# Kernel optimization log

Hardware: AMD Instinct MI355X
Metric: run time of the kernel (lower is better)

Reference implementation:

```python
import jax, jax.numpy as jnp
import numpy as np

N_NODES = 65536
N_EDGES = 262144
N_GRAPHS = 2048
NF = 16   # num_node_features
EF = 6    # num_edge_features
H1, H2, H3 = 32, 16, 8  # conv1 out, conv2 out, lin1 out


def _lin_init(key, fan_in, fan_out):
    kw, kb = jax.random.split(key)
    s = 1.0 / np.sqrt(fan_in)
    w = jax.random.uniform(kw, (fan_in, fan_out), minval=-s, maxval=s, dtype=jnp.float32)
    b = jax.random.uniform(kb, (fan_out,), minval=-s, maxval=s, dtype=jnp.float32)
    return w, b


def setup_inputs() -> dict:
    key = jax.random.key(0)
    ks = jax.random.split(key, 16)
    inp = {}
    inp["x_p"] = jax.random.normal(ks[0], (N_NODES, NF), dtype=jnp.float32)
    inp["x_d"] = jax.random.normal(ks[1], (4, NF), dtype=jnp.float32)  # unused by forward
    inp["edge_attr_p"] = jax.random.uniform(ks[2], (N_EDGES, EF), dtype=jnp.float32)
    inp["edge_attr_d"] = jax.random.uniform(ks[3], (4, EF), dtype=jnp.float32)  # unused
    inp["edge_index_p"] = jax.random.randint(ks[4], (2, N_EDGES), 0, N_NODES, dtype=jnp.int32)
    inp["x_p_batch"] = jnp.sort(jax.random.randint(ks[5], (N_NODES,), 0, N_GRAPHS, dtype=jnp.int32))
    # conv1: NNConv(NF, 32); edge nn: Linear(EF,16) -> ReLU -> Linear(16, NF*32)
    inp["nn1_w1"], inp["nn1_b1"] = _lin_init(ks[6], EF, 16)
    inp["nn1_w2"], inp["nn1_b2"] = _lin_init(ks[7], 16, NF * H1)
    inp["root1"] = _lin_init(ks[8], NF, H1)[0]
    inp["bias1"] = jnp.zeros((H1,), dtype=jnp.float32)
    # conv2: NNConv(32, 16); edge nn: Linear(EF,16) -> ReLU -> Linear(16, 32*16)
    inp["nn2_w1"], inp["nn2_b1"] = _lin_init(ks[9], EF, 16)
    inp["nn2_w2"], inp["nn2_b2"] = _lin_init(ks[10], 16, H1 * H2)
    inp["root2"] = _lin_init(ks[11], H1, H2)[0]
    inp["bias2"] = jnp.zeros((H2,), dtype=jnp.float32)
    # attention pooling gate: Linear(NF,NF) -> ReLU -> Linear(NF,1)
    inp["gate_w1"], inp["gate_b1"] = _lin_init(ks[12], NF, NF)
    inp["gate_w2"], inp["gate_b2"] = _lin_init(ks[13], NF, 1)
    # head: Linear(16+16, 8) -> Linear(8, 1)  (attention=True)
    inp["lin1_w"], inp["lin1_b"] = _lin_init(ks[14], H2 + NF, H3)
    inp["lin2_w"], inp["lin2_b"] = _lin_init(ks[15], H3, 1)
    return inp


def _nnconv(x, edge_attr, src, dst, w1, b1, w2, b2, root, bias, in_c, out_c, n_nodes):
    # per-edge dynamic weight matrix Theta(e) : [E, in_c, out_c]
    h = jax.nn.relu(edge_attr @ w1 + b1) @ w2 + b2
    w_dyn = h.reshape(-1, in_c, out_c)
    msg = jnp.einsum('ei,eio->eo', x[src], w_dyn)          # [E, out_c]
    agg = jax.ops.segment_sum(msg, dst, num_segments=n_nodes)  # scatter-add
    return agg + x @ root + bias


def _attention_pool(x, batch, gw1, gb1, gw2, gb2, n_graphs):
    g = (jax.nn.relu(x @ gw1 + gb1) @ gw2 + gb2)[:, 0]     # [N] gate logits
    m = jax.ops.segment_max(g, batch, num_segments=n_graphs)
    e = jnp.exp(g - m[batch])
    s = jax.ops.segment_sum(e, batch, num_segments=n_graphs)
    alpha = e / s[batch]                                    # per-graph softmax
    return jax.ops.segment_sum(alpha[:, None] * x, batch, num_segments=n_graphs)


def _mean_pool(x, batch, n_graphs):
    s = jax.ops.segment_sum(x, batch, num_segments=n_graphs)
    cnt = jax.ops.segment_sum(jnp.ones((x.shape[0],), x.dtype), batch, num_segments=n_graphs)
    return s / jnp.maximum(cnt, 1.0)[:, None]


def reference(x_p, x_d, edge_attr_p, edge_attr_d, edge_index_p, x_p_batch,
              nn1_w1, nn1_b1, nn1_w2, nn1_b2, root1, bias1,
              nn2_w1, nn2_b1, nn2_w2, nn2_b2, root2, bias2,
              gate_w1, gate_b1, gate_w2, gate_b2,
              lin1_w, lin1_b, lin2_w, lin2_b):
    src, dst = edge_index_p[0], edge_index_p[1]
    # attention pooling on raw node features (attention=True)
    x_att = _attention_pool(x_p, x_p_batch, gate_w1, gate_b1, gate_w2, gate_b2, N_GRAPHS)
    # two NNConv layers with ReLU
    h = jax.nn.relu(_nnconv(x_p, edge_attr_p, src, dst, nn1_w1, nn1_b1, nn1_w2, nn1_b2,
                            root1, bias1, NF, H1, N_NODES))
    h = jax.nn.relu(_nnconv(h, edge_attr_p, src, dst, nn2_w1, nn2_b1, nn2_w2, nn2_b2,
                            root2, bias2, H1, H2, N_NODES))
    g = _mean_pool(h, x_p_batch, N_GRAPHS)                  # [B, 16]
    g = jnp.concatenate([g, x_att], axis=1)                 # [B, 32]
    # dropout p=0.5 is identity in eval mode
    g = g @ lin1_w + lin1_b
    out = g @ lin2_w + lin2_b                               # [B, 1]
    return out
```

## Files before the change

### kernel.cpp

```cpp
#include <hip/hip_runtime.h>

#define NN 65536
#define NE 262144
#define NG 2048

typedef __attribute__((ext_vector_type(16))) float f32x16;
typedef __attribute__((ext_vector_type(4)))  float f32x4;
typedef __attribute__((ext_vector_type(8)))  __bf16 bf16x8;

__device__ inline unsigned pack2(float a, float b) {
    return __builtin_amdgcn_perm(__float_as_uint(b), __float_as_uint(a), 0x07060302u);
}
__device__ inline float lof(float p) {
    return p - __uint_as_float(__float_as_uint(p) & 0xffff0000u);
}
__device__ inline bf16x8 asb(uint4 u) { return __builtin_bit_cast(bf16x8, u); }

__global__ __launch_bounds__(256) void k_setup(
    const int* __restrict__ batch,
    const float* __restrict__ w2a, const float* __restrict__ b2a,
    const float* __restrict__ w2b, const float* __restrict__ b2c,
    int* __restrict__ cnt, int* __restrict__ cur, int* __restrict__ goffs,
    unsigned* __restrict__ f1, unsigned* __restrict__ f2)
{
    int t = blockIdx.x * 256 + threadIdx.x;
    if (t < NN) { cnt[t] = 0; cur[t] = 0; }
    if (t <= NG) {
        int lo = 0, hi = NN;
        while (lo < hi) {
            int mid = (lo + hi) >> 1;
            if (batch[mid] < t) lo = mid + 1; else hi = mid;
        }
        goffs[t] = lo;
    }
    if (t < 17408) {
        int c = t / 8704;
        int r = t - c * 8704;
        int d = r & 3;
        int l = (r >> 2) & 63;
        int tt = (r >> 8) & 1;
        int s = r >> 9;
        if (c == 0) {
            int n = l & 31, g = l >> 5;
            int j0 = 2*d;
            int c0 = (g*8 + j0)*32 + n;
            int c1 = c0 + 32;
            float a = (s < 16) ? w2a[s*512 + c0] : b2a[c0];
            float b = (s < 16) ? w2a[s*512 + c1] : b2a[c1];
            f1[r] = tt ? pack2(lof(a), lof(b)) : pack2(a, b);
        } else {
            int n = l & 15, g = l >> 4;
            int j0 = 2*d;
            int c0 = (g*8 + j0)*16 + n;
            int c1 = c0 + 16;
            float a = (s < 16) ? w2b[s*512 + c0] : b2c[c0];
            float b = (s < 16) ? w2b[s*512 + c1] : b2c[c1];
            f2[r] = tt ? pack2(lof(a), lof(b)) : pack2(a, b);
        }
    }
}

__global__ __launch_bounds__(64) void k_gateatt(const float* __restrict__ x,
    const float* __restrict__ gw1, const float* __restrict__ gb1,
    const float* __restrict__ gw2, const float* __restrict__ gb2,
    const int* __restrict__ goffs, float* __restrict__ x_att)
{
    __shared__ float sw[256];
    __shared__ float sb[16];
    __shared__ float sw2[16];
    __shared__ float sb2;
    __shared__ float gb[1024];
    const int g = blockIdx.x;
    const int lane = threadIdx.x;
    for (int i = lane; i < 256; i += 64) sw[i] = gw1[i];
    if (lane < 16) { sb[lane] = gb1[lane]; sw2[lane] = gw2[lane]; }
    if (lane == 0) sb2 = gb2[0];
    const int s = goffs[g], e = goffs[g + 1];
    const int cnt = e - s;
    if (cnt <= 0) {
        if (lane < 16) x_att[g*16 + lane] = 0.f;
        return;
    }
    const int cap = cnt < 1024 ? cnt : 1024;
    __syncthreads();
    for (int ii = lane; ii < cap; ii += 64) {
        const float4* xp = (const float4*)(x + (size_t)(s + ii) * 16);
        float xv[16];
#pragma unroll
        for (int i = 0; i < 4; ++i) {
            float4 tt = xp[i];
            xv[4*i] = tt.x; xv[4*i+1] = tt.y; xv[4*i+2] = tt.z; xv[4*i+3] = tt.w;
        }
        float gv = sb2;
#pragma unroll
        for (int j = 0; j < 16; ++j) {
            float a = sb[j];
#pragma unroll
            for (int i = 0; i < 16; ++i) a += xv[i] * sw[i*16 + j];
            gv += fmaxf(a, 0.f) * sw2[j];
        }
        gb[ii] = gv;
    }
    __syncthreads();
    float m = -1e30f;
    for (int ii = lane; ii < cap; ii += 64) m = fmaxf(m, gb[ii]);
#pragma unroll
    for (int d = 32; d; d >>= 1) m = fmaxf(m, __shfl_xor(m, d));
    float sum = 0.f;
    for (int ii = lane; ii < cap; ii += 64) {
        float ev = expf(gb[ii] - m);
        gb[ii] = ev;
        sum += ev;
    }
#pragma unroll
    for (int d = 32; d; d >>= 1) sum += __shfl_xor(sum, d);
    const float inv = 1.f / sum;
    __syncthreads();
    const int f = lane & 15, sub = lane >> 4;
    float acc = 0.f;
    for (int ii = sub; ii < cap; ii += 4)
        acc += gb[ii] * inv * x[(size_t)(s + ii)*16 + f];
    acc += __shfl_xor(acc, 16);
    acc += __shfl_xor(acc, 32);
    if (lane < 16) x_att[g*16 + f] = acc;
}

__global__ __launch_bounds__(256) void k_hist(const int* __restrict__ ei, int* __restrict__ cnt)
{
    int e = blockIdx.x * 256 + threadIdx.x;
    if (e >= NE) return;
    atomicAdd(&cnt[ei[NE + e]], 1);
}

__global__ __launch_bounds__(256) void k_scan_blk(const int* __restrict__ cnt,
    int* __restrict__ offs, int* __restrict__ bsum)
{
    __shared__ int s[256];
    int t = threadIdx.x, b = blockIdx.x;
    int v = cnt[b*256 + t];
    s[t] = v;
    __syncthreads();
#pragma unroll
    for (int d = 1; d < 256; d <<= 1) {
        int add = (t >= d) ? s[t - d] : 0;
        __syncthreads();
        s[t] += add;
        __syncthreads();
    }
    offs[b*256 + t] = s[t] - v;
    if (t == 255) bsum[b] = s[255];
}

__global__ __launch_bounds__(256) void k_scan_top(const int* __restrict__ bsum,
    int* __restrict__ boff)
{
    __shared__ int s[256];
    int t = threadIdx.x;
    int v = bsum[t];
    s[t] = v;
    __syncthreads();
#pragma unroll
    for (int d = 1; d < 256; d <<= 1) {
        int add = (t >= d) ? s[t - d] : 0;
        __syncthreads();
        s[t] += add;
        __syncthreads();
    }
    boff[t] = s[t] - v;
}

__global__ __launch_bounds__(256) void k_scan_add(int* __restrict__ offs,
    const int* __restrict__ boff)
{
    int i = blockIdx.x * 256 + threadIdx.x;
    if (i == 0) offs[NN] = NE;
    if (i >= NN) return;
    offs[i] += boff[i >> 8];
}

__global__ __launch_bounds__(256) void k_scatter(const int* __restrict__ ei,
    const int* __restrict__ offs, int* __restrict__ cur, int2* __restrict__ epair)
{
    int e = blockIdx.x * 256 + threadIdx.x;
    if (e >= NE) return;
    int d = ei[NE + e];
    int pos = offs[d] + atomicAdd(&cur[d], 1);
    epair[pos] = make_int2(e, ei[e]);
}

__global__ __launch_bounds__(256) void k_conv1(
    const float* __restrict__ x, const float* __restrict__ ea,
    const int2* __restrict__ epair,
    const float* __restrict__ w1, const float* __restrict__ b1,
    const unsigned* __restrict__ bfrag, float* __restrict__ msg)
{
    __shared__ uint4 s_tab[17*2*64];
    const int tid  = threadIdx.x;
    for (int i = tid; i < 17*2*64; i += 256) s_tab[i] = ((const uint4*)bfrag)[i];
    __syncthreads();
    const int lane = tid & 63;
    const int wid  = tid >> 6;
    const int m    = lane & 31;
    const int g    = lane >> 5;

    const int tile = blockIdx.x*4 + wid;
    const int p    = tile*32 + m;
    const int2 ep  = epair[p];
    const int e    = ep.x, src = ep.y;

    float xs[8];
    {
        const float4* xp = (const float4*)(x + (size_t)src*16 + g*8);
        float4 aa = xp[0], bb = xp[1];
        xs[0]=aa.x; xs[1]=aa.y; xs[2]=aa.z; xs[3]=aa.w;
        xs[4]=bb.x; xs[5]=bb.y; xs[6]=bb.z; xs[7]=bb.w;
    }
    float h[17];
    {
        const float2 e01 = *(const float2*)(ea + (size_t)e*6);
        const float2 e23 = *(const float2*)(ea + (size_t)e*6 + 2);
        const float2 e45 = *(const float2*)(ea + (size_t)e*6 + 4);
        const float a0=e01.x, a1=e01.y, a2=e23.x, a3=e23.y, a4=e45.x, a5=e45.y;
#pragma unroll
        for (int j = 0; j < 16; ++j) {
            float c = b1[j];
            c += a0*w1[0*16+j]; c += a1*w1[1*16+j]; c += a2*w1[2*16+j];
            c += a3*w1[3*16+j]; c += a4*w1[4*16+j]; c += a5*w1[5*16+j];
            h[j] = fmaxf(c, 0.f);
        }
        h[16] = 1.f;
    }

    f32x16 acc0 = {}, acc1 = {};
#pragma unroll
    for (int s = 0; s < 17; ++s) {
        const float hs = h[s];
        float p0 = hs*xs[0], p1 = hs*xs[1], p2 = hs*xs[2], p3 = hs*xs[3];
        float p4 = hs*xs[4], p5 = hs*xs[5], p6 = hs*xs[6], p7 = hs*xs[7];
        uint4 uh = { pack2(p0,p1), pack2(p2,p3), pack2(p4,p5), pack2(p6,p7) };
        uint4 ul = { pack2(lof(p0),lof(p1)), pack2(lof(p2),lof(p3)),
                     pack2(lof(p4),lof(p5)), pack2(lof(p6),lof(p7)) };
        uint4 wh = s_tab[(s*2+0)*64 + lane];
        uint4 wl = s_tab[(s*2+1)*64 + lane];
        if (s & 1) {
            acc1 = __builtin_amdgcn_mfma_f32_32x32x16_bf16(asb(uh), asb(wh), acc1, 0, 0, 0);
            acc1 = __builtin_amdgcn_mfma_f32_32x32x16_bf16(asb(uh), asb(wl), acc1, 0, 0, 0);
            acc1 = __builtin_amdgcn_mfma_f32_32x32x16_bf16(asb(ul), asb(wh), acc1, 0, 0, 0);
        } else {
            acc0 = __builtin_amdgcn_mfma_f32_32x32x16_bf16(asb(uh), asb(wh), acc0, 0, 0, 0);
            acc0 = __builtin_amdgcn_mfma_f32_32x32x16_bf16(asb(uh), asb(wl), acc0, 0, 0, 0);
            acc0 = __builtin_amdgcn_mfma_f32_32x32x16_bf16(asb(ul), asb(wh), acc0, 0, 0, 0);
        }
    }

    float* mbase = msg + (size_t)tile*32*32;
    const int rb = g*4;
#pragma unroll
    for (int r = 0; r < 16; ++r) {
        int mr = (r&3) + 8*(r>>2) + rb;
        mbase[(size_t)mr*32 + m] = acc0[r] + acc1[r];
    }
}

__global__ __launch_bounds__(256) void k_conv2(
    const float* __restrict__ x, const float* __restrict__ ea,
    const int2* __restrict__ epair,
    const float* __restrict__ w1, const float* __restrict__ b1,
    const unsigned* __restrict__ bfrag, float* __restrict__ msg)
{
    __shared__ uint4 s_tab[17*2*64];
    __shared__ float lt[4][16*21];
    const int tid  = threadIdx.x;
    for (int i = tid; i < 17*2*64; i += 256) s_tab[i] = ((const uint4*)bfrag)[i];
    __syncthreads();
    const int lane = tid & 63;
    const int wid  = tid >> 6;
    const int m    = lane & 15;
    const int g    = lane >> 4;

    const int tile = blockIdx.x*4 + wid;
    const int p    = tile*16 + m;
    const int2 ep  = epair[p];
    const int e    = ep.x, src = ep.y;

    uint4 xh, xl;
    {
        const float4* xp = (const float4*)(x + (size_t)src*32 + g*8);
        float4 aa = xp[0], bb = xp[1];
        xh = (uint4){ pack2(aa.x,aa.y), pack2(aa.z,aa.w), pack2(bb.x,bb.y), pack2(bb.z,bb.w) };
        xl = (uint4){ pack2(lof(aa.x),lof(aa.y)), pack2(lof(aa.z),lof(aa.w)),
                      pack2(lof(bb.x),lof(bb.y)), pack2(lof(bb.z),lof(bb.w)) };
    }
    float h[17];
    {
        const float2 e01 = *(const float2*)(ea + (size_t)e*6);
        const float2 e23 = *(const float2*)(ea + (size_t)e*6 + 2);
        const float2 e45 = *(const float2*)(ea + (size_t)e*6 + 4);
        const float a0=e01.x, a1=e01.y, a2=e23.x, a3=e23.y, a4=e45.x, a5=e45.y;
#pragma unroll
        for (int j = 0; j < 16; ++j) {
            float c = b1[j];
            c += a0*w1[0*16+j]; c += a1*w1[1*16+j]; c += a2*w1[2*16+j];
            c += a3*w1[3*16+j]; c += a4*w1[4*16+j]; c += a5*w1[5*16+j];
            h[j] = fmaxf(c, 0.f);
        }
        h[16] = 1.f;
    }

    f32x4 macc = {};
#pragma unroll
    for (int s = 0; s < 17; ++s) {
        uint4 wh = s_tab[(s*2+0)*64 + lane];
        uint4 wl = s_tab[(s*2+1)*64 + lane];
        f32x4 t = {};
        t = __builtin_amdgcn_mfma_f32_16x16x32_bf16(asb(wh), asb(xh), t, 0, 0, 0);
        t = __builtin_amdgcn_mfma_f32_16x16x32_bf16(asb(wl), asb(xh), t, 0, 0, 0);
        t = __builtin_amdgcn_mfma_f32_16x16x32_bf16(asb(wh), asb(xl), t, 0, 0, 0);
        const float hs = h[s];
        macc.x += hs*t.x; macc.y += hs*t.y; macc.z += hs*t.z; macc.w += hs*t.w;
    }

    float* lw = lt[wid];
    lw[m*21 + g*4 + 0] = macc.x;
    lw[m*21 + g*4 + 1] = macc.y;
    lw[m*21 + g*4 + 2] = macc.z;
    lw[m*21 + g*4 + 3] = macc.w;
    asm volatile("s_waitcnt lgkmcnt(0)" ::: "memory");
    const int rrow = lane >> 2, fq = lane & 3;
    float o0 = lw[rrow*21 + fq*4 + 0];
    float o1 = lw[rrow*21 + fq*4 + 1];
    float o2 = lw[rrow*21 + fq*4 + 2];
    float o3 = lw[rrow*21 + fq*4 + 3];
    float4* mb = (float4*)(msg + (size_t)tile*256);
    mb[rrow*4 + fq] = make_float4(o0, o1, o2, o3);
}

__global__ __launch_bounds__(256) void k_reduce1(
    const float* __restrict__ msg, const int* __restrict__ offs,
    const float* __restrict__ x, const float* __restrict__ root,
    const float* __restrict__ bias, float* __restrict__ h1)
{
    __shared__ float s_r[512];
    __shared__ float s_b[32];
    int tid = threadIdx.x;
    for (int i = tid; i < 512; i += 256) s_r[i] = root[i];
    if (tid < 32) s_b[tid] = bias[tid];
    __syncthreads();
    int gid = blockIdx.x * 256 + tid;
    int n = gid >> 3, q = gid & 7;
    int s = offs[n], e = offs[n + 1];
    float4 acc = make_float4(s_b[4*q], s_b[4*q+1], s_b[4*q+2], s_b[4*q+3]);
    const float4* s_r4 = (const float4*)s_r;
    const float* xp = x + (size_t)n * 16;
#pragma unroll
    for (int i = 0; i < 16; ++i) {
        float xi = xp[i];
        float4 w = s_r4[i*8 + q];
        acc.x += xi*w.x; acc.y += xi*w.y; acc.z += xi*w.z; acc.w += xi*w.w;
    }
    for (int p = s; p < e; ++p) {
        float4 mr = ((const float4*)(msg + (size_t)p * 32))[q];
        acc.x += mr.x; acc.y += mr.y; acc.z += mr.z; acc.w += mr.w;
    }
    acc.x = fmaxf(acc.x, 0.f); acc.y = fmaxf(acc.y, 0.f);
    acc.z = fmaxf(acc.z, 0.f); acc.w = fmaxf(acc.w, 0.f);
    ((float4*)(h1 + (size_t)n * 32))[q] = acc;
}

__global__ __launch_bounds__(256) void k_reduce2(
    const float* __restrict__ msg, const int* __restrict__ offs,
    const float* __restrict__ h1, const float* __restrict__ root,
    const float* __restrict__ bias, float* __restrict__ h2)
{
    __shared__ float s_r[512];
    __shared__ float s_b[16];
    int tid = threadIdx.x;
    for (int i = tid; i < 512; i += 256) s_r[i] = root[i];
    if (tid < 16) s_b[tid] = bias[tid];
    __syncthreads();
    int gid = blockIdx.x * 256 + tid;
    int n = gid >> 2, q = gid & 3;
    int s = offs[n], e = offs[n + 1];
    float4 acc = make_float4(s_b[4*q], s_b[4*q+1], s_b[4*q+2], s_b[4*q+3]);
    const float4* s_r4 = (const float4*)s_r;
    const float* xp = h1 + (size_t)n * 32;
#pragma unroll
    for (int i = 0; i < 32; ++i) {
        float xi = xp[i];
        float4 w = s_r4[i*4 + q];
        acc.x += xi*w.x; acc.y += xi*w.y; acc.z += xi*w.z; acc.w += xi*w.w;
    }
    for (int p = s; p < e; ++p) {
        float4 mr = ((const float4*)(msg + (size_t)p * 16))[q];
        acc.x += mr.x; acc.y += mr.y; acc.z += mr.z; acc.w += mr.w;
    }
    acc.x = fmaxf(acc.x, 0.f); acc.y = fmaxf(acc.y, 0.f);
    acc.z = fmaxf(acc.z, 0.f); acc.w = fmaxf(acc.w, 0.f);
    ((float4*)(h2 + (size_t)n * 16))[q] = acc;
}

__global__ __launch_bounds__(64) void k_head(
    const float* __restrict__ h2, const float* __restrict__ x_att,
    const int* __restrict__ goffs,
    const float* __restrict__ l1w, const float* __restrict__ l1b,
    const float* __restrict__ l2w, const float* __restrict__ l2b,
    float* __restrict__ out)
{
    int g = blockIdx.x;
    int lane = threadIdx.x;
    int s = goffs[g], e = goffs[g + 1];
    __shared__ float v[32];
    __shared__ float hmid[8];
    int f = lane & 15, sub = lane >> 4;
    float acc = 0.f;
    for (int i = s + sub; i < e; i += 4) acc += h2[(size_t)i*16 + f];
    acc += __shfl_xor(acc, 16);
    acc += __shfl_xor(acc, 32);
    float cnt = fmaxf((float)(e - s), 1.0f);
    if (lane < 16) {
        v[lane]      = acc / cnt;
        v[16 + lane] = x_att[g*16 + lane];
    }
    __syncthreads();
    if (lane < 8) {
        float a = l1b[lane];
#pragma unroll
        for (int i = 0; i < 32; ++i) a += v[i] * l1w[i*8 + lane];
        hmid[lane] = a;
    }
    __syncthreads();
    if (lane == 0) {
        float a = l2b[0];
#pragma unroll
        for (int j = 0; j < 8; ++j) a += hmid[j] * l2w[j];
        out[g] = a;
    }
}

extern "C" void kernel_launch(void* const* d_in, const int* in_sizes, int n_in,
                              void* d_out, int out_size, void* d_ws, size_t ws_size,
                              hipStream_t stream) {
    const float* x_p    = (const float*)d_in[0];
    const float* ea_p   = (const float*)d_in[2];
    const int*   ei     = (const int*)d_in[4];
    const int*   batch  = (const int*)d_in[5];
    const float* nn1_w1 = (const float*)d_in[6];
    const float* nn1_b1 = (const float*)d_in[7];
    const float* nn1_w2 = (const float*)d_in[8];
    const float* nn1_b2 = (const float*)d_in[9];
    const float* root1  = (const float*)d_in[10];
    const float* bias1  = (const float*)d_in[11];
    const float* nn2_w1 = (const float*)d_in[12];
    const float* nn2_b1 = (const float*)d_in[13];
    const float* nn2_w2 = (const float*)d_in[14];
    const float* nn2_b2 = (const float*)d_in[15];
    const float* root2  = (const float*)d_in[16];
    const float* bias2  = (const float*)d_in[17];
    const float* gw1    = (const float*)d_in[18];
    const float* gb1    = (const float*)d_in[19];
    const float* gw2    = (const float*)d_in[20];
    const float* gb2    = (const float*)d_in[21];
    const float* l1w    = (const float*)d_in[22];
    const float* l1b    = (const float*)d_in[23];
    const float* l2w    = (const float*)d_in[24];
    const float* l2b    = (const float*)d_in[25];

    float*    h1     = (float*)d_ws;
    float*    h2     = h1 + (size_t)NN * 32;
    float*    x_att  = h2 + (size_t)NN * 16;
    int*      goffs  = (int*)(x_att + (size_t)NG * 16);
    int*      offs   = goffs + 2052;
    int*      cnt    = offs + 65540;
    int*      cur    = cnt + NN;
    int*      bsum   = cur + NN;
    int*      boff   = bsum + 256;
    int2*     epair  = (int2*)(boff + 256);
    unsigned* bfrag1 = (unsigned*)(epair + NE);
    unsigned* bfrag2 = bfrag1 + 8704;
    float*    msg    = (float*)(bfrag2 + 8704);

    k_setup<<<512, 256, 0, stream>>>(batch, nn1_w2, nn1_b2, nn2_w2, nn2_b2,
                                     cnt, cur, goffs, bfrag1, bfrag2);

    k_gateatt<<<NG, 64, 0, stream>>>(x_p, gw1, gb1, gw2, gb2, goffs, x_att);

    k_hist<<<NE/256, 256, 0, stream>>>(ei, cnt);
    k_scan_blk<<<NN/256, 256, 0, stream>>>(cnt, offs, bsum);
    k_scan_top<<<1, 256, 0, stream>>>(bsum, boff);
    k_scan_add<<<NN/256, 256, 0, stream>>>(offs, boff);
    k_scatter<<<NE/256, 256, 0, stream>>>(ei, offs, cur, epair);

    k_conv1<<<2048, 256, 0, stream>>>(x_p, ea_p, epair, nn1_w1, nn1_b1, bfrag1, msg);
    k_reduce1<<<NN*8/256, 256, 0, stream>>>(msg, offs, x_p, root1, bias1, h1);

    k_conv2<<<4096, 256, 0, stream>>>(h1, ea_p, epair, nn2_w1, nn2_b1, bfrag2, msg);
    k_reduce2<<<NN*4/256, 256, 0, stream>>>(msg, offs, h1, root2, bias2, h2);

    k_head<<<NG, 64, 0, stream>>>(h2, x_att, goffs, l1w, l1b, l2w, l2b, (float*)d_out);
}
```

Measured before the change: 136.4 us.

## Fuse all stages into one persistent cooperative kernel with grid syncs

Measured after the change: 454.9 us. 3.33x slower.

```diff
diff --git a/kernel.cpp b/kernel.cpp
--- a/kernel.cpp
+++ b/kernel.cpp
@@ -1,8 +1,12 @@
 #include <hip/hip_runtime.h>
+#include <hip/hip_cooperative_groups.h>
+
+namespace cg = cooperative_groups;
 
 #define NN 65536
 #define NE 262144
 #define NG 2048
+#define NTHR 256
 
 typedef __attribute__((ext_vector_type(16))) float f32x16;
 typedef __attribute__((ext_vector_type(4)))  float f32x4;
@@ -15,6 +19,406 @@
     return p - __uint_as_float(__float_as_uint(p) & 0xffff0000u);
 }
 __device__ inline bf16x8 asb(uint4 u) { return __builtin_bit_cast(bf16x8, u); }
+__device__ inline void wave_lds_fence() {
+    asm volatile("s_waitcnt lgkmcnt(0)" ::: "memory");
+}
+
+struct Params {
+    const float *x, *ea;
+    const int *ei, *batch;
+    const float *w1a, *b1a, *w2a, *b2a, *roota, *biasa;
+    const float *w1b, *b1b, *w2b, *b2b, *rootb, *biasb;
+    const float *gw1, *gb1, *gw2, *gb2;
+    const float *l1w, *l1b, *l2w, *l2b;
+    float *out;
+    float *h1, *h2, *x_att;
+    int *goffs, *offs, *cnt, *cur, *bsum, *boff;
+    int2 *epair;
+    unsigned *f1, *f2;
+    float *msg;
+};
+
+__global__ __launch_bounds__(256, 2) void k_all(Params P)
+{
+    cg::grid_group grid = cg::this_grid();
+    __shared__ __align__(16) char smem[34816];
+    const int tid   = threadIdx.x;
+    const int bid   = blockIdx.x;
+    const int gsz   = gridDim.x * NTHR;
+    const int nwave = gridDim.x * 4;
+    const int gtid  = bid*NTHR + tid;
+    const int lane  = tid & 63;
+    const int wid   = tid >> 6;
+    const int gwave = bid*4 + wid;
+
+    for (int t = gtid; t < 131072; t += gsz) {
+        if (t < NN) { P.cnt[t] = 0; P.cur[t] = 0; }
+        if (t <= NG) {
+            int lo = 0, hi = NN;
+            while (lo < hi) {
+                int mid = (lo + hi) >> 1;
+                if (P.batch[mid] < t) lo = mid + 1; else hi = mid;
+            }
+            P.goffs[t] = lo;
+        }
+        if (t < 17408) {
+            int c = t / 8704;
+            int r = t - c * 8704;
+            int d = r & 3;
+            int l = (r >> 2) & 63;
+            int tt = (r >> 8) & 1;
+            int s = r >> 9;
+            if (c == 0) {
+                int n = l & 31, g = l >> 5;
+                int j0 = 2*d;
+                int c0 = (g*8 + j0)*32 + n;
+                int c1 = c0 + 32;
+                float a = (s < 16) ? P.w2a[s*512 + c0] : P.b2a[c0];
+                float b = (s < 16) ? P.w2a[s*512 + c1] : P.b2a[c1];
+                P.f1[r] = tt ? pack2(lof(a), lof(b)) : pack2(a, b);
+            } else {
+                int n = l & 15, g = l >> 4;
+                int j0 = 2*d;
+                int c0 = (g*8 + j0)*16 + n;
+                int c1 = c0 + 16;
+                float a = (s < 16) ? P.w2b[s*512 + c0] : P.b2b[c0];
+                float b = (s < 16) ? P.w2b[s*512 + c1] : P.b2b[c1];
+                P.f2[r] = tt ? pack2(lof(a), lof(b)) : pack2(a, b);
+            }
+        }
+    }
+    grid.sync();
+
+    {
+        for (int e = gtid; e < NE; e += gsz)
+            atomicAdd(&P.cnt[P.ei[NE + e]], 1);
+
+        float* sgb = (float*)smem;
+        float* sw  = (float*)(smem + 16384);
+        float* sb  = sw + 256;
+        float* sw2 = sb + 16;
+        float* sb2 = sw2 + 16;
+        if (tid < 256) sw[tid] = P.gw1[tid];
+        if (tid < 16) { sb[tid] = P.gb1[tid]; sw2[tid] = P.gw2[tid]; }
+        if (tid == 0) sb2[0] = P.gb2[0];
+        __syncthreads();
+
+        float* gb = sgb + wid*1024;
+        for (int g = gwave; g < NG; g += nwave) {
+            const int s = P.goffs[g], e = P.goffs[g + 1];
+            const int cntg = e - s;
+            if (cntg <= 0) {
+                if (lane < 16) P.x_att[g*16 + lane] = 0.f;
+                continue;
+            }
+            const int cap = cntg < 1024 ? cntg : 1024;
+            for (int ii = lane; ii < cap; ii += 64) {
+                const float4* xp = (const float4*)(P.x + (size_t)(s + ii) * 16);
+                float xv[16];
+#pragma unroll
+                for (int i = 0; i < 4; ++i) {
+                    float4 t4 = xp[i];
+                    xv[4*i] = t4.x; xv[4*i+1] = t4.y; xv[4*i+2] = t4.z; xv[4*i+3] = t4.w;
+                }
+                float gv = sb2[0];
+#pragma unroll
+                for (int j = 0; j < 16; ++j) {
+                    float a = sb[j];
+#pragma unroll
+                    for (int i = 0; i < 16; ++i) a += xv[i] * sw[i*16 + j];
+                    gv += fmaxf(a, 0.f) * sw2[j];
+                }
+                gb[ii] = gv;
+            }
+            wave_lds_fence();
+            float m = -1e30f;
+            for (int ii = lane; ii < cap; ii += 64) m = fmaxf(m, gb[ii]);
+#pragma unroll
+            for (int d = 32; d; d >>= 1) m = fmaxf(m, __shfl_xor(m, d));
+            float sum = 0.f;
+            for (int ii = lane; ii < cap; ii += 64) {
+                float ev = expf(gb[ii] - m);
+                gb[ii] = ev;
+                sum += ev;
+            }
+#pragma unroll
+            for (int d = 32; d; d >>= 1) sum += __shfl_xor(sum, d);
+            const float inv = 1.f / sum;
+            wave_lds_fence();
+            const int f = lane & 15, sub = lane >> 4;
+            float acc = 0.f;
+            for (int ii = sub; ii < cap; ii += 4)
+                acc += gb[ii] * inv * P.x[(size_t)(s + ii)*16 + f];
+            acc += __shfl_xor(acc, 16);
+            acc += __shfl_xor(acc, 32);
+            if (lane < 16) P.x_att[g*16 + f] = acc;
+            wave_lds_fence();
+        }
+    }
+    grid.sync();
+
+    {
+        int* s = (int*)smem;
+        for (int c = bid; c < 256; c += gridDim.x) {
+            int v = P.cnt[c*256 + tid];
+            __syncthreads();
+            s[tid] = v;
+            __syncthreads();
+#pragma unroll
+            for (int d = 1; d < 256; d <<= 1) {
+                int add = (tid >= d) ? s[tid - d] : 0;
+                __syncthreads();
+                s[tid] += add;
+                __syncthreads();
+            }
+            P.offs[c*256 + tid] = s[tid] - v;
+            if (tid == 255) P.bsum[c] = s[255];
+        }
+    }
+    grid.sync();
+
+    if (bid == 0) {
+        int* s = (int*)smem;
+        int v = P.bsum[tid];
+        __syncthreads();
+        s[tid] = v;
+        __syncthreads();
+#pragma unroll
+        for (int d = 1; d < 256; d <<= 1) {
+            int add = (tid >= d) ? s[tid - d] : 0;
+            __syncthreads();
+            s[tid] += add;
+            __syncthreads();
+        }
+        P.boff[tid] = s[tid] - v;
+    }
+    grid.sync();
+
+    for (int i = gtid; i < NN; i += gsz) P.offs[i] += P.boff[i >> 8];
+    if (gtid == 0) P.offs[NN] = NE;
+    grid.sync();
+
+    for (int e = gtid; e < NE; e += gsz) {
+        int d = P.ei[NE + e];
+        int pos = P.offs[d] + atomicAdd(&P.cur[d], 1);
+        P.epair[pos] = make_int2(e, P.ei[e]);
+    }
+    grid.sync();
+
+    {
+        uint4* tab = (uint4*)smem;
+        __syncthreads();
+        for (int i = tid; i < 2176; i += 256) tab[i] = ((const uint4*)P.f1)[i];
+        __syncthreads();
+        const int m = lane & 31, g8 = lane >> 5;
+        for (int tile = gwave; tile < NE/32; tile += nwave) {
+            const int p = tile*32 + m;
+            const int2 ep = P.epair[p];
+            const int e = ep.x, src = ep.y;
+            float xs[8];
+            {
+                const float4* xp = (const float4*)(P.x + (size_t)src*16 + g8*8);
+                float4 aa = xp[0], bb = xp[1];
+                xs[0]=aa.x; xs[1]=aa.y; xs[2]=aa.z; xs[3]=aa.w;
+                xs[4]=bb.x; xs[5]=bb.y; xs[6]=bb.z; xs[7]=bb.w;
+            }
+            float h[17];
+            {
+                const float2 e01 = *(const float2*)(P.ea + (size_t)e*6);
+                const float2 e23 = *(const float2*)(P.ea + (size_t)e*6 + 2);
+                const float2 e45 = *(const float2*)(P.ea + (size_t)e*6 + 4);
+                const float a0=e01.x, a1=e01.y, a2=e23.x, a3=e23.y, a4=e45.x, a5=e45.y;
+#pragma unroll
+                for (int j = 0; j < 16; ++j) {
+                    float c = P.b1a[j];
+                    c += a0*P.w1a[0*16+j]; c += a1*P.w1a[1*16+j]; c += a2*P.w1a[2*16+j];
+                    c += a3*P.w1a[3*16+j]; c += a4*P.w1a[4*16+j]; c += a5*P.w1a[5*16+j];
+                    h[j] = fmaxf(c, 0.f);
+                }
+                h[16] = 1.f;
+            }
+            f32x16 acc0 = {}, acc1 = {};
+#pragma unroll
+            for (int s = 0; s < 17; ++s) {
+                const float hs = h[s];
+                float p0 = hs*xs[0], p1 = hs*xs[1], p2 = hs*xs[2], p3 = hs*xs[3];
+                float p4 = hs*xs[4], p5 = hs*xs[5], p6 = hs*xs[6], p7 = hs*xs[7];
+                uint4 uh = { pack2(p0,p1), pack2(p2,p3), pack2(p4,p5), pack2(p6,p7) };
+                uint4 ul = { pack2(lof(p0),lof(p1)), pack2(lof(p2),lof(p3)),
+                             pack2(lof(p4),lof(p5)), pack2(lof(p6),lof(p7)) };
+                uint4 wh = tab[(s*2+0)*64 + lane];
+                uint4 wl = tab[(s*2+1)*64 + lane];
+                if (s & 1) {
+                    acc1 = __builtin_amdgcn_mfma_f32_32x32x16_bf16(asb(uh), asb(wh), acc1, 0, 0, 0);
+                    acc1 = __builtin_amdgcn_mfma_f32_32x32x16_bf16(asb(uh), asb(wl), acc1, 0, 0, 0);
+                    acc1 = __builtin_amdgcn_mfma_f32_32x32x16_bf16(asb(ul), asb(wh), acc1, 0, 0, 0);
+                } else {
+                    acc0 = __builtin_amdgcn_mfma_f32_32x32x16_bf16(asb(uh), asb(wh), acc0, 0, 0, 0);
+                    acc0 = __builtin_amdgcn_mfma_f32_32x32x16_bf16(asb(uh), asb(wl), acc0, 0, 0, 0);
+                    acc0 = __builtin_amdgcn_mfma_f32_32x32x16_bf16(asb(ul), asb(wh), acc0, 0, 0, 0);
+                }
+            }
+            float* mbase = P.msg + (size_t)tile*32*32;
+            const int rb = g8*4;
+#pragma unroll
+            for (int r = 0; r < 16; ++r) {
+                int mr = (r&3) + 8*(r>>2) + rb;
+                mbase[(size_t)mr*32 + m] = acc0[r] + acc1[r];
+            }
+        }
+    }
+    grid.sync();
+
+    {
+        float* s_r = (float*)smem;
+        float* s_b = s_r + 512;
+        __syncthreads();
+        for (int i = tid; i < 512; i += 256) s_r[i] = P.roota[i];
+        if (tid < 32) s_b[tid] = P.biasa[tid];
+        __syncthreads();
+        const float4* s_r4 = (const float4*)s_r;
+        for (int gid = gtid; gid < NN*8; gid += gsz) {
+            int n = gid >> 3, q = gid & 7;
+            int s = P.offs[n], e = P.offs[n + 1];
+            float4 acc = make_float4(s_b[4*q], s_b[4*q+1], s_b[4*q+2], s_b[4*q+3]);
+            const float* xp = P.x + (size_t)n * 16;
+#pragma unroll
+            for (int i = 0; i < 16; ++i) {
+                float xi = xp[i];
+                float4 w = s_r4[i*8 + q];
+                acc.x += xi*w.x; acc.y += xi*w.y; acc.z += xi*w.z; acc.w += xi*w.w;
+            }
+            for (int p = s; p < e; ++p) {
+                float4 mr = ((const float4*)(P.msg + (size_t)p * 32))[q];
+                acc.x += mr.x; acc.y += mr.y; acc.z += mr.z; acc.w += mr.w;
+            }
+            acc.x = fmaxf(acc.x, 0.f); acc.y = fmaxf(acc.y, 0.f);
+            acc.z = fmaxf(acc.z, 0.f); acc.w = fmaxf(acc.w, 0.f);
+            ((float4*)(P.h1 + (size_t)n * 32))[q] = acc;
+        }
+    }
+    grid.sync();
+
+    {
+        uint4* tab = (uint4*)smem;
+        __syncthreads();
+        for (int i = tid; i < 2176; i += 256) tab[i] = ((const uint4*)P.f2)[i];
+        __syncthreads();
+        const int m = lane & 15, g8 = lane >> 4;
+        const int srcl = (lane & 3) * 16 + (lane >> 2);
+        for (int tile = gwave; tile < NE/16; tile += nwave) {
+            const int p = tile*16 + m;
+            const int2 ep = P.epair[p];
+            const int e = ep.x, src = ep.y;
+            uint4 xh, xl;
+            {
+                const float4* xp = (const float4*)(P.h1 + (size_t)src*32 + g8*8);
+                float4 aa = xp[0], bb = xp[1];
+                xh = (uint4){ pack2(aa.x,aa.y), pack2(aa.z,aa.w), pack2(bb.x,bb.y), pack2(bb.z,bb.w) };
+                xl = (uint4){ pack2(lof(aa.x),lof(aa.y)), pack2(lof(aa.z),lof(aa.w)),
+                              pack2(lof(bb.x),lof(bb.y)), pack2(lof(bb.z),lof(bb.w)) };
+            }
+            float h[17];
+            {
+                const float2 e01 = *(const float2*)(P.ea + (size_t)e*6);
+                const float2 e23 = *(const float2*)(P.ea + (size_t)e*6 + 2);
+                const float2 e45 = *(const float2*)(P.ea + (size_t)e*6 + 4);
+                const float a0=e01.x, a1=e01.y, a2=e23.x, a3=e23.y, a4=e45.x, a5=e45.y;
+#pragma unroll
+                for (int j = 0; j < 16; ++j) {
+                    float c = P.b1b[j];
+                    c += a0*P.w1b[0*16+j]; c += a1*P.w1b[1*16+j]; c += a2*P.w1b[2*16+j];
+                    c += a3*P.w1b[3*16+j]; c += a4*P.w1b[4*16+j]; c += a5*P.w1b[5*16+j];
+                    h[j] = fmaxf(c, 0.f);
+                }
+                h[16] = 1.f;
+            }
+            f32x4 macc = {};
+#pragma unroll
+            for (int s = 0; s < 17; ++s) {
+                uint4 wh = tab[(s*2+0)*64 + lane];
+                uint4 wl = tab[(s*2+1)*64 + lane];
+                f32x4 t = {};
+                t = __builtin_amdgcn_mfma_f32_16x16x32_bf16(asb(wh), asb(xh), t, 0, 0, 0);
+                t = __builtin_amdgcn_mfma_f32_16x16x32_bf16(asb(wl), asb(xh), t, 0, 0, 0);
+                t = __builtin_amdgcn_mfma_f32_16x16x32_bf16(asb(wh), asb(xl), t, 0, 0, 0);
+                const float hs = h[s];
+                macc.x += hs*t.x; macc.y += hs*t.y; macc.z += hs*t.z; macc.w += hs*t.w;
+            }
+            float o0 = __shfl(macc.x, srcl);
+            float o1 = __shfl(macc.y, srcl);
+            float o2 = __shfl(macc.z, srcl);
+            float o3 = __shfl(macc.w, srcl);
+            float4* mb = (float4*)(P.msg + (size_t)tile*256);
+            mb[lane] = make_float4(o0, o1, o2, o3);
+        }
+    }
+    grid.sync();
+
+    {
+        float* s_r = (float*)smem;
+        float* s_b = s_r + 512;
+        __syncthreads();
+        for (int i = tid; i < 512; i += 256) s_r[i] = P.rootb[i];
+        if (tid < 16) s_b[tid] = P.biasb[tid];
+        __syncthreads();
+        const float4* s_r4 = (const float4*)s_r;
+        for (int gid = gtid; gid < NN*4; gid += gsz) {
+            int n = gid >> 2, q = gid & 3;
+            int s = P.offs[n], e = P.offs[n + 1];
+            float4 acc = make_float4(s_b[4*q], s_b[4*q+1], s_b[4*q+2], s_b[4*q+3]);
+            const float* xp = P.h1 + (size_t)n * 32;
+#pragma unroll
+            for (int i = 0; i < 32; ++i) {
+                float xi = xp[i];
+                float4 w = s_r4[i*4 + q];
+                acc.x += xi*w.x; acc.y += xi*w.y; acc.z += xi*w.z; acc.w += xi*w.w;
+            }
+            for (int p = s; p < e; ++p) {
+                float4 mr = ((const float4*)(P.msg + (size_t)p * 16))[q];
+                acc.x += mr.x; acc.y += mr.y; acc.z += mr.z; acc.w += mr.w;
+            }
+            acc.x = fmaxf(acc.x, 0.f); acc.y = fmaxf(acc.y, 0.f);
+            acc.z = fmaxf(acc.z, 0.f); acc.w = fmaxf(acc.w, 0.f);
+            ((float4*)(P.h2 + (size_t)n * 16))[q] = acc;
+        }
+    }
+    grid.sync();
+
+    {
+        float* v = (float*)smem + wid*64;
+        float* hmid = v + 32;
+        __syncthreads();
+        for (int g = gwave; g < NG; g += nwave) {
+            const int s = P.goffs[g], e = P.goffs[g + 1];
+            const int f = lane & 15, sub = lane >> 4;
+            float acc = 0.f;
+            for (int i = s + sub; i < e; i += 4) acc += P.h2[(size_t)i*16 + f];
+            acc += __shfl_xor(acc, 16);
+            acc += __shfl_xor(acc, 32);
+            float cntg = fmaxf((float)(e - s), 1.0f);
+            if (lane < 16) {
+                v[lane]      = acc / cntg;
+                v[16 + lane] = P.x_att[g*16 + lane];
+            }
+            wave_lds_fence();
+            if (lane < 8) {
+                float a = P.l1b[lane];
+#pragma unroll
+                for (int i = 0; i < 32; ++i) a += v[i] * P.l1w[i*8 + lane];
+                hmid[lane] = a;
+            }
+            wave_lds_fence();
+            if (lane == 0) {
+                float a = P.l2b[0];
+#pragma unroll
+                for (int j = 0; j < 8; ++j) a += hmid[j] * P.l2w[j];
+                P.out[g] = a;
+            }
+            wave_lds_fence();
+        }
+    }
+}
 
 __global__ __launch_bounds__(256) void k_setup(
     const int* __restrict__ batch,
@@ -325,7 +729,7 @@
     lw[m*21 + g*4 + 1] = macc.y;
     lw[m*21 + g*4 + 2] = macc.z;
     lw[m*21 + g*4 + 3] = macc.w;
-    asm volatile("s_waitcnt lgkmcnt(0)" ::: "memory");
+    wave_lds_fence();
     const int rrow = lane >> 2, fq = lane & 3;
     float o0 = lw[rrow*21 + fq*4 + 0];
     float o1 = lw[rrow*21 + fq*4 + 1];
@@ -440,61 +844,79 @@
 extern "C" void kernel_launch(void* const* d_in, const int* in_sizes, int n_in,
                               void* d_out, int out_size, void* d_ws, size_t ws_size,
                               hipStream_t stream) {
-    const float* x_p    = (const float*)d_in[0];
-    const float* ea_p   = (const float*)d_in[2];
-    const int*   ei     = (const int*)d_in[4];
-    const int*   batch  = (const int*)d_in[5];
-    const float* nn1_w1 = (const float*)d_in[6];
-    const float* nn1_b1 = (const float*)d_in[7];
-    const float* nn1_w2 = (const float*)d_in[8];
-    const float* nn1_b2 = (const float*)d_in[9];
-    const float* root1  = (const float*)d_in[10];
-    const float* bias1  = (const float*)d_in[11];
-    const float* nn2_w1 = (const float*)d_in[12];
-    const float* nn2_b1 = (const float*)d_in[13];
-    const float* nn2_w2 = (const float*)d_in[14];
-    const float* nn2_b2 = (const float*)d_in[15];
-    const float* root2  = (const float*)d_in[16];
-    const float* bias2  = (const float*)d_in[17];
-    const float* gw1    = (const float*)d_in[18];
-    const float* gb1    = (const float*)d_in[19];
-    const float* gw2    = (const float*)d_in[20];
-    const float* gb2    = (const float*)d_in[21];
-    const float* l1w    = (const float*)d_in[22];
-    const float* l1b    = (const float*)d_in[23];
-    const float* l2w    = (const float*)d_in[24];
-    const float* l2b    = (const float*)d_in[25];
-
-    float*    h1     = (float*)d_ws;
-    float*    h2     = h1 + (size_t)NN * 32;
-    float*    x_att  = h2 + (size_t)NN * 16;
-    int*      goffs  = (int*)(x_att + (size_t)NG * 16);
-    int*      offs   = goffs + 2052;
-    int*      cnt    = offs + 65540;
-    int*      cur    = cnt + NN;
-    int*      bsum   = cur + NN;
-    int*      boff   = bsum + 256;
-    int2*     epair  = (int2*)(boff + 256);
-    unsigned* bfrag1 = (unsigned*)(epair + NE);
-    unsigned* bfrag2 = bfrag1 + 8704;
-    float*    msg    = (float*)(bfrag2 + 8704);
-
-    k_setup<<<512, 256, 0, stream>>>(batch, nn1_w2, nn1_b2, nn2_w2, nn2_b2,
-                                     cnt, cur, goffs, bfrag1, bfrag2);
-
-    k_gateatt<<<NG, 64, 0, stream>>>(x_p, gw1, gb1, gw2, gb2, goffs, x_att);
-
-    k_hist<<<NE/256, 256, 0, stream>>>(ei, cnt);
+    Params P;
+    P.x     = (const float*)d_in[0];
+    P.ea    = (const float*)d_in[2];
+    P.ei    = (const int*)d_in[4];
+    P.batch = (const int*)d_in[5];
+    P.w1a   = (const float*)d_in[6];
+    P.b1a   = (const float*)d_in[7];
+    P.w2a   = (const float*)d_in[8];
+    P.b2a   = (const float*)d_in[9];
+    P.roota = (const float*)d_in[10];
+    P.biasa = (const float*)d_in[11];
+    P.w1b   = (const float*)d_in[12];
+    P.b1b   = (const float*)d_in[13];
+    P.w2b   = (const float*)d_in[14];
+    P.b2b   = (const float*)d_in[15];
+    P.rootb = (const float*)d_in[16];
+    P.biasb = (const float*)d_in[17];
+    P.gw1   = (const float*)d_in[18];
+    P.gb1   = (const float*)d_in[19];
+    P.gw2   = (const float*)d_in[20];
+    P.gb2   = (const float*)d_in[21];
+    P.l1w   = (const float*)d_in[22];
+    P.l1b   = (const float*)d_in[23];
+    P.l2w   = (const float*)d_in[24];
+    P.l2b   = (const float*)d_in[25];
+    P.out   = (float*)d_out;
+
+    float* h1    = (float*)d_ws;
+    float* h2    = h1 + (size_t)NN * 32;
+    float* x_att = h2 + (size_t)NN * 16;
+    int*   goffs = (int*)(x_att + (size_t)NG * 16);
+    int*   offs  = goffs + 2052;
+    int*   cnt   = offs + 65540;
+    int*   cur   = cnt + NN;
+    int*   bsum  = cur + NN;
+    int*   boff  = bsum + 256;
+    int2*  epair = (int2*)(boff + 256);
+    unsigned* f1 = (unsigned*)(epair + NE);
+    unsigned* f2 = f1 + 8704;
+    float* msg   = (float*)(f2 + 8704);
+
+    P.h1 = h1; P.h2 = h2; P.x_att = x_att;
+    P.goffs = goffs; P.offs = offs; P.cnt = cnt; P.cur = cur;
+    P.bsum = bsum; P.boff = boff;
+    P.epair = epair; P.f1 = f1; P.f2 = f2; P.msg = msg;
+
+    int dev = 0;
+    (void)hipGetDevice(&dev);
+    int coopSupported = 0, nCU = 0, occ = 0;
+    (void)hipDeviceGetAttribute(&coopSupported, hipDeviceAttributeCooperativeLaunch, dev);
+    (void)hipDeviceGetAttribute(&nCU, hipDeviceAttributeMultiprocessorCount, dev);
+    (void)hipOccupancyMaxActiveBlocksPerMultiprocessor(&occ, k_all, NTHR, 0);
+
+    if (coopSupported && occ >= 1 && nCU >= 1) {
+        long long grid = (long long)occ * nCU;
+        if (grid > 512) grid = 512;
+        void* args[] = { &P };
+        hipError_t err = hipLaunchCooperativeKernel((const void*)k_all,
+                              dim3((unsigned)grid), dim3(NTHR), args, 0, stream);
+        if (err == hipSuccess) return;
+    }
+
+    k_setup<<<512, 256, 0, stream>>>(P.batch, P.w2a, P.b2a, P.w2b, P.b2b,
+                                     cnt, cur, goffs, f1, f2);
+    k_gateatt<<<NG, 64, 0, stream>>>(P.x, P.gw1, P.gb1, P.gw2, P.gb2, goffs, x_att);
+    k_hist<<<NE/256, 256, 0, stream>>>(P.ei, cnt);
     k_scan_blk<<<NN/256, 256, 0, stream>>>(cnt, offs, bsum);
     k_scan_top<<<1, 256, 0, stream>>>(bsum, boff);
     k_scan_add<<<NN/256, 256, 0, stream>>>(offs, boff);
-    k_scatter<<<NE/256, 256, 0, stream>>>(ei, offs, cur, epair);
-
-    k_conv1<<<2048, 256, 0, stream>>>(x_p, ea_p, epair, nn1_w1, nn1_b1, bfrag1, msg);
-    k_reduce1<<<NN*8/256, 256, 0, stream>>>(msg, offs, x_p, root1, bias1, h1);
-
-    k_conv2<<<4096, 256, 0, stream>>>(h1, ea_p, epair, nn2_w1, nn2_b1, bfrag2, msg);
-    k_reduce2<<<NN*4/256, 256, 0, stream>>>(msg, offs, h1, root2, bias2, h2);
-
-    k_head<<<NG, 64, 0, stream>>>(h2, x_att, goffs, l1w, l1b, l2w, l2b, (float*)d_out);
-}
+    k_scatter<<<NE/256, 256, 0, stream>>>(P.ei, offs, cur, epair);
+    k_conv1<<<2048, 256, 0, stream>>>(P.x, P.ea, epair, P.w1a, P.b1a, f1, msg);
+    k_reduce1<<<NN*8/256, 256, 0, stream>>>(msg, offs, P.x, P.roota, P.biasa, h1);
+    k_conv2<<<4096, 256, 0, stream>>>(h1, P.ea, epair, P.w1b, P.b1b, f2, msg);
+    k_reduce2<<<NN*4/256, 256, 0, stream>>>(msg, offs, h1, P.rootb, P.biasb, h2);
+    k_head<<<NG, 64, 0, stream>>>(h2, x_att, goffs, P.l1w, P.l1b, P.l2w, P.l2b, P.out);
+}
```
